# Kernel tuning notes

Hardware: AMD Instinct MI355X
Metric: run time of the kernel (lower is better)

## Reference

```python
import jax, jax.numpy as jnp
import numpy as np

N = 8192          # number of nodes
IN_F = 256        # in_features
OUT_F = 128       # out_features
ALPHA = 0.2       # LeakyReLU negative slope


def setup_inputs() -> dict:
    key = jax.random.key(0)
    k1, k2, k3, k4 = jax.random.split(key, 4)
    h = jax.random.normal(k1, (N, IN_F), dtype=jnp.float32)
    adj = jax.random.randint(k2, (N, N), 0, 2, dtype=jnp.int32)  # dense 0/1 adjacency mask
    W = (jax.random.normal(k3, (IN_F, OUT_F), dtype=jnp.float32) * 0.05)   # W.weight^T
    a = (jax.random.normal(k4, (2 * OUT_F,), dtype=jnp.float32) * 0.05)    # a.weight flattened
    return {"h": h, "adj": adj, "W": W, "a": a}


def reference(h, adj, W, a):
    # Wh = self.W(h): [N, OUT_F]
    Wh = h @ W
    # Original builds an [N, N, 2F] concat tensor then projects with 'a'.
    # Equivalent math: e[i, j] = leaky_relu(Wh[i]@a1 + Wh[j]@a2)
    a1, a2 = a[:OUT_F], a[OUT_F:]
    src = Wh @ a1                                     # [N] per-source score
    dst = Wh @ a2                                     # [N] per-target score
    e = jax.nn.leaky_relu(src[:, None] + dst[None, :], negative_slope=ALPHA)  # [N, N]
    # masked softmax over neighbors (dim=1); adj==0 -> -inf
    e = jnp.where(adj == 0, -jnp.inf, e)
    attention = jax.nn.softmax(e, axis=1)             # [N, N]
    # dropout p=0 in eval-mode reference -> identity
    h_prime = attention @ Wh                          # [N, OUT_F]
    return jax.nn.elu(h_prime)                        # concat=True -> ELU
```

## Files before the change

### kernel.cpp

```cpp
#include <hip/hip_runtime.h>
#include <math.h>

#define N 8192
#define IN_F 256
#define OUT_F 128
#define ALPHA 0.2f
#define JS 8
#define NSTEP 32

typedef _Float16 f16;
typedef __attribute__((ext_vector_type(4))) float f32x4;
typedef __attribute__((ext_vector_type(8))) _Float16 f16x8;
typedef __attribute__((ext_vector_type(4))) _Float16 f16x4;

__global__ __launch_bounds__(256) void k_prep(const float* __restrict__ W,
                                              f16* __restrict__ WT) {
    int idx = blockIdx.x * 256 + threadIdx.x;
    int f = idx >> 8;
    int k = idx & 255;
    WT[idx] = (f16)W[k * OUT_F + f];
}

#define HS 280
__global__ __launch_bounds__(256) void k_wh(const float* __restrict__ h,
                                            const f16* __restrict__ WT,
                                            const float* __restrict__ a,
                                            f16* __restrict__ WhT,
                                            float* __restrict__ src,
                                            float* __restrict__ dst) {
    __shared__ __align__(16) f16 hA[32][HS];
    __shared__ __align__(16) f16 outT[128][40];
    __shared__ float sred[4][32], dred[4][32];

    const int t = threadIdx.x;
    const int i0 = blockIdx.x * 32;
    const int wv = t >> 6, l = t & 63, ln = l & 15, lq = l >> 4;

    {
        const float4* hg = (const float4*)(h + (size_t)i0 * IN_F);
#pragma unroll
        for (int it = 0; it < 8; ++it) {
            int idx = t + it * 256;
            int r = idx >> 6;
            int c4 = (idx & 63) * 4;
            float4 v = hg[idx];
            f16x4 p = { (f16)v.x, (f16)v.y, (f16)v.z, (f16)v.w };
            *(f16x4*)&hA[r][c4] = p;
        }
    }
    __syncthreads();

    f32x4 acc00 = {0.f,0.f,0.f,0.f}, acc01 = {0.f,0.f,0.f,0.f};
    f32x4 acc10 = {0.f,0.f,0.f,0.f}, acc11 = {0.f,0.f,0.f,0.f};
    const int f0 = 32 * wv;

#pragma unroll
    for (int ks = 0; ks < 8; ++ks) {
        const int k0 = 32 * ks + 8 * lq;
        f16x8 a0 = *(const f16x8*)&hA[ln][k0];
        f16x8 a1 = *(const f16x8*)&hA[16 + ln][k0];
        f16x8 b0 = *(const f16x8*)(WT + (size_t)(f0 + ln) * IN_F + k0);
        f16x8 b1 = *(const f16x8*)(WT + (size_t)(f0 + 16 + ln) * IN_F + k0);
        acc00 = __builtin_amdgcn_mfma_f32_16x16x32_f16(a0, b0, acc00, 0, 0, 0);
        acc01 = __builtin_amdgcn_mfma_f32_16x16x32_f16(a0, b1, acc01, 0, 0, 0);
        acc10 = __builtin_amdgcn_mfma_f32_16x16x32_f16(a1, b0, acc10, 0, 0, 0);
        acc11 = __builtin_amdgcn_mfma_f32_16x16x32_f16(a1, b1, acc11, 0, 0, 0);
    }

    const float a1c0 = a[f0 + ln],      a2c0 = a[128 + f0 + ln];
    const float a1c1 = a[f0 + 16 + ln], a2c1 = a[128 + f0 + 16 + ln];
    float sp[8], dp[8];
#pragma unroll
    for (int i = 0; i < 8; ++i) { sp[i] = 0.f; dp[i] = 0.f; }

#pragma unroll
    for (int hh = 0; hh < 2; ++hh) {
        f32x4 v0 = hh ? acc10 : acc00;
        f32x4 v1 = hh ? acc11 : acc01;
        f16x4 p0, p1;
#pragma unroll
        for (int rg = 0; rg < 4; ++rg) {
            sp[hh * 4 + rg] += v0[rg] * a1c0 + v1[rg] * a1c1;
            dp[hh * 4 + rg] += v0[rg] * a2c0 + v1[rg] * a2c1;
            p0[rg] = (f16)v0[rg];
            p1[rg] = (f16)v1[rg];
        }
        *(f16x4*)&outT[f0 + ln][16 * hh + 4 * lq] = p0;
        *(f16x4*)&outT[f0 + 16 + ln][16 * hh + 4 * lq] = p1;
    }
#pragma unroll
    for (int i = 0; i < 8; ++i) {
        float s = sp[i], d = dp[i];
        s += __shfl_down(s, 8, 16); d += __shfl_down(d, 8, 16);
        s += __shfl_down(s, 4, 16); d += __shfl_down(d, 4, 16);
        s += __shfl_down(s, 2, 16); d += __shfl_down(d, 2, 16);
        s += __shfl_down(s, 1, 16); d += __shfl_down(d, 1, 16);
        if (ln == 0) {
            int row = 16 * (i >> 2) + 4 * lq + (i & 3);
            sred[wv][row] = s;
            dred[wv][row] = d;
        }
    }
    __syncthreads();
    if (t < 32) {
        src[i0 + t] = sred[0][t] + sred[1][t] + sred[2][t] + sred[3][t];
        dst[i0 + t] = dred[0][t] + dred[1][t] + dred[2][t] + dred[3][t];
    }
    {
        const int col = t & 127, g = t >> 7;
        const int ct = i0 >> 7, jo = i0 & 127;
        f16x8 q0 = *(const f16x8*)&outT[col][16 * g];
        f16x8 q1 = *(const f16x8*)&outT[col][16 * g + 8];
        f16* dstp = WhT + (size_t)ct * (128 * 128) + (size_t)col * 128 + jo + 16 * g;
        *(f16x8*)(dstp) = q0;
        *(f16x8*)(dstp + 8) = q1;
    }
}

__global__ __launch_bounds__(256, 2) void k_attn(const int* __restrict__ adj,
                                                 const f16* __restrict__ WhT,
                                                 const float* __restrict__ src,
                                                 const float* __restrict__ dst,
                                                 float* __restrict__ p_part,
                                                 float* __restrict__ l_part) {
    const int t = threadIdx.x;
    const int wv = t >> 6, l = t & 63, ln = l & 15, lq = l >> 4;
    const int i0 = (blockIdx.x * 4 + wv) * 32;
    const int jq = blockIdx.y;
    const int jbase = jq * (N / JS);

    const float src0 = src[i0 + ln];
    const float src1 = src[i0 + 16 + ln];
    const float c0 = fabsf(src0) + 4.0f;
    const float c1 = fabsf(src1) + 4.0f;
    float lp0 = 0.f, lp1 = 0.f;

    f32x4 acc0[8], acc1[8];
#pragma unroll
    for (int ft = 0; ft < 8; ++ft) {
        acc0[ft] = (f32x4){0.f,0.f,0.f,0.f};
        acc1[ft] = (f32x4){0.f,0.f,0.f,0.f};
    }

    const int* arow0 = adj + (size_t)(i0 + ln) * N + jbase + 8 * lq;
    const int* arow1 = arow0 + (size_t)16 * N;
    const float* drow = dst + jbase + 8 * lq;
    const f16* Bb = WhT + (size_t)(jq * 8) * (128 * 128) + (size_t)ln * 128 + 8 * lq;

    int4 pa0[2][2], pa1[2][2];
    float4 pd[2][2];

    auto issue = [&](int s, int p) {
        const int off = 32 * (s & (NSTEP - 1));
        pa0[p][0] = *(const int4*)(arow0 + off);
        pa0[p][1] = *(const int4*)(arow0 + off + 4);
        pa1[p][0] = *(const int4*)(arow1 + off);
        pa1[p][1] = *(const int4*)(arow1 + off + 4);
        pd[p][0]  = *(const float4*)(drow + off);
        pd[p][1]  = *(const float4*)(drow + off + 4);
    };

    issue(0, 0);
    issue(1, 1);

#pragma unroll 4
    for (int s = 0; s < NSTEP; ++s) {
        const int p = s & 1;
        const int4 a00 = pa0[p][0], a01 = pa0[p][1];
        const int4 a10 = pa1[p][0], a11 = pa1[p][1];
        const float4 d0 = pd[p][0], d1 = pd[p][1];
        issue(s + 2, p);

        const int* av0 = (const int*)&a00;
        const int* av1 = (const int*)&a01;
        const int* bv0 = (const int*)&a10;
        const int* bv1 = (const int*)&a11;
        const float* df0 = (const float*)&d0;
        const float* df1 = (const float*)&d1;

        f16x8 af0, af1;
#pragma unroll
        for (int k = 0; k < 4; ++k) {
            float e0 = src0 + df0[k];
            float w0 = av0[k] ? __expf(fmaxf(e0, ALPHA * e0) - c0) : 0.f;
            lp0 += w0; af0[k] = (f16)w0;
            float e1 = src1 + df0[k];
            float w1 = bv0[k] ? __expf(fmaxf(e1, ALPHA * e1) - c1) : 0.f;
            lp1 += w1; af1[k] = (f16)w1;
        }
#pragma unroll
        for (int k = 0; k < 4; ++k) {
            float e0 = src0 + df1[k];
            float w0 = av1[k] ? __expf(fmaxf(e0, ALPHA * e0) - c0) : 0.f;
            lp0 += w0; af0[4 + k] = (f16)w0;
            float e1 = src1 + df1[k];
            float w1 = bv1[k] ? __expf(fmaxf(e1, ALPHA * e1) - c1) : 0.f;
            lp1 += w1; af1[4 + k] = (f16)w1;
        }

        const f16* bp = Bb + (s >> 2) * (128 * 128) + (s & 3) * 32;
#pragma unroll
        for (int ft = 0; ft < 8; ++ft) {
            f16x8 bf = *(const f16x8*)(bp + ft * (16 * 128));
            acc0[ft] = __builtin_amdgcn_mfma_f32_16x16x32_f16(af0, bf, acc0[ft], 0, 0, 0);
            acc1[ft] = __builtin_amdgcn_mfma_f32_16x16x32_f16(af1, bf, acc1[ft], 0, 0, 0);
        }
    }

    lp0 += __shfl_down(lp0, 32); lp0 += __shfl_down(lp0, 16);
    lp1 += __shfl_down(lp1, 32); lp1 += __shfl_down(lp1, 16);
    if (l < 16) {
        l_part[(size_t)jq * N + i0 + l] = lp0;
        l_part[(size_t)jq * N + i0 + 16 + l] = lp1;
    }

    float* pb = p_part + (size_t)jq * N * OUT_F;
#pragma unroll
    for (int ft = 0; ft < 8; ++ft) {
#pragma unroll
        for (int rg = 0; rg < 4; ++rg) {
            pb[(size_t)(i0 + 4 * lq + rg) * OUT_F + 16 * ft + ln] = acc0[ft][rg];
            pb[(size_t)(i0 + 16 + 4 * lq + rg) * OUT_F + 16 * ft + ln] = acc1[ft][rg];
        }
    }
}

__global__ __launch_bounds__(256) void k_comb(const float* __restrict__ p_part,
                                              const float* __restrict__ l_part,
                                              float* __restrict__ out) {
    const int idx4 = blockIdx.x * 256 + threadIdx.x;
    const int row = idx4 >> 5;
    const float4* pp = (const float4*)p_part;
    float4 p = pp[idx4];
    float lsum = l_part[row];
#pragma unroll
    for (int q = 1; q < JS; ++q) {
        float4 v = pp[(size_t)q * (N * OUT_F / 4) + idx4];
        p.x += v.x; p.y += v.y; p.z += v.z; p.w += v.w;
        lsum += l_part[(size_t)q * N + row];
    }
    float inv = 1.0f / lsum;
    float4 r;
    r.x = p.x * inv; r.x = r.x > 0.f ? r.x : expm1f(r.x);
    r.y = p.y * inv; r.y = r.y > 0.f ? r.y : expm1f(r.y);
    r.z = p.z * inv; r.z = r.z > 0.f ? r.z : expm1f(r.z);
    r.w = p.w * inv; r.w = r.w > 0.f ? r.w : expm1f(r.w);
    ((float4*)out)[idx4] = r;
}

extern "C" void kernel_launch(void* const* d_in, const int* in_sizes, int n_in,
                              void* d_out, int out_size, void* d_ws, size_t ws_size,
                              hipStream_t stream) {
    const float* h   = (const float*)d_in[0];
    const int*   adj = (const int*)d_in[1];
    const float* W   = (const float*)d_in[2];
    const float* a   = (const float*)d_in[3];
    float* out = (float*)d_out;

    char* ws = (char*)d_ws;
    f16*   WT     = (f16*)ws;                       ws += 64 * 1024;
    f16*   WhT    = (f16*)ws;                       ws += 2 * 1024 * 1024;
    float* src    = (float*)ws;                     ws += N * sizeof(float);
    float* dst    = (float*)ws;                     ws += N * sizeof(float);
    float* l_part = (float*)ws;                     ws += (size_t)JS * N * sizeof(float);
    float* p_part = (float*)ws;

    k_prep<<<128, 256, 0, stream>>>(W, WT);
    k_wh<<<N / 32, 256, 0, stream>>>(h, WT, a, WhT, src, dst);
    dim3 agrid(N / 128, JS);
    k_attn<<<agrid, 256, 0, stream>>>(adj, WhT, src, dst, p_part, l_part);
    k_comb<<<N * OUT_F / 4 / 256, 256, 0, stream>>>(p_part, l_part, out);
}
```

Before: 443.4 us.

## Pack adjacency into bitmask in pre-pass and prefetch WhT fragments in attention loop

Adds a pre-pass kernel that compresses the int32 adjacency matrix into a bitmask, so the attention kernel reads 1 bit per edge instead of 4 bytes. The attention loop now loads mask words per 4-step group and double-buffers the WhT B-fragments in registers one step ahead. The full 256 MB adjacency still has to be read once by the pack kernel, which adds a launch and a workspace buffer. It also raises register pressure in the attention kernel.

```diff
diff --git a/kernel.cpp b/kernel.cpp
--- a/kernel.cpp
+++ b/kernel.cpp
@@ -7,6 +7,7 @@
 #define ALPHA 0.2f
 #define JS 8
 #define NSTEP 32
+#define MW (N / 32)
 
 typedef _Float16 f16;
 typedef __attribute__((ext_vector_type(4))) float f32x4;
@@ -19,6 +20,24 @@
     int f = idx >> 8;
     int k = idx & 255;
     WT[idx] = (f16)W[k * OUT_F + f];
+}
+
+__global__ __launch_bounds__(256) void k_pack(const int* __restrict__ adj,
+                                              unsigned* __restrict__ M) {
+    const int t = threadIdx.x;
+    const int l = t & 63;
+    const size_t tot = (size_t)N * N / 4;
+    const size_t stride = (size_t)gridDim.x * 256;
+    size_t idx = (size_t)blockIdx.x * 256 + t;
+    const int4* ap = (const int4*)adj;
+    for (; idx < tot; idx += stride) {
+        int4 v = ap[idx];
+        unsigned m = (v.x ? 1u : 0u) | (v.y ? 2u : 0u) | (v.z ? 4u : 0u) | (v.w ? 8u : 0u);
+        m |= __shfl_down(m, 1) << 4;
+        m |= __shfl_down(m, 2) << 8;
+        m |= __shfl_down(m, 4) << 16;
+        if ((l & 7) == 0) M[idx >> 3] = m;
+    }
 }
 
 #define HS 280
@@ -117,7 +136,7 @@
     }
 }
 
-__global__ __launch_bounds__(256, 2) void k_attn(const int* __restrict__ adj,
+__global__ __launch_bounds__(256, 2) void k_attn(const unsigned* __restrict__ M,
                                                  const f16* __restrict__ WhT,
                                                  const float* __restrict__ src,
                                                  const float* __restrict__ dst,
@@ -142,69 +161,68 @@
         acc1[ft] = (f32x4){0.f,0.f,0.f,0.f};
     }
 
-    const int* arow0 = adj + (size_t)(i0 + ln) * N + jbase + 8 * lq;
-    const int* arow1 = arow0 + (size_t)16 * N;
+    const unsigned* Mr0 = M + (size_t)(i0 + ln) * MW + jq * (NSTEP);
+    const unsigned* Mr1 = Mr0 + (size_t)16 * MW;
     const float* drow = dst + jbase + 8 * lq;
     const f16* Bb = WhT + (size_t)(jq * 8) * (128 * 128) + (size_t)ln * 128 + 8 * lq;
 
-    int4 pa0[2][2], pa1[2][2];
     float4 pd[2][2];
-
-    auto issue = [&](int s, int p) {
+    auto dissue = [&](int s, int p) {
         const int off = 32 * (s & (NSTEP - 1));
-        pa0[p][0] = *(const int4*)(arow0 + off);
-        pa0[p][1] = *(const int4*)(arow0 + off + 4);
-        pa1[p][0] = *(const int4*)(arow1 + off);
-        pa1[p][1] = *(const int4*)(arow1 + off + 4);
-        pd[p][0]  = *(const float4*)(drow + off);
-        pd[p][1]  = *(const float4*)(drow + off + 4);
+        pd[p][0] = *(const float4*)(drow + off);
+        pd[p][1] = *(const float4*)(drow + off + 4);
     };
-
-    issue(0, 0);
-    issue(1, 1);
-
-#pragma unroll 4
-    for (int s = 0; s < NSTEP; ++s) {
-        const int p = s & 1;
-        const int4 a00 = pa0[p][0], a01 = pa0[p][1];
-        const int4 a10 = pa1[p][0], a11 = pa1[p][1];
-        const float4 d0 = pd[p][0], d1 = pd[p][1];
-        issue(s + 2, p);
-
-        const int* av0 = (const int*)&a00;
-        const int* av1 = (const int*)&a01;
-        const int* bv0 = (const int*)&a10;
-        const int* bv1 = (const int*)&a11;
-        const float* df0 = (const float*)&d0;
-        const float* df1 = (const float*)&d1;
-
-        f16x8 af0, af1;
-#pragma unroll
-        for (int k = 0; k < 4; ++k) {
-            float e0 = src0 + df0[k];
-            float w0 = av0[k] ? __expf(fmaxf(e0, ALPHA * e0) - c0) : 0.f;
-            lp0 += w0; af0[k] = (f16)w0;
-            float e1 = src1 + df0[k];
-            float w1 = bv0[k] ? __expf(fmaxf(e1, ALPHA * e1) - c1) : 0.f;
-            lp1 += w1; af1[k] = (f16)w1;
-        }
-#pragma unroll
-        for (int k = 0; k < 4; ++k) {
-            float e0 = src0 + df1[k];
-            float w0 = av1[k] ? __expf(fmaxf(e0, ALPHA * e0) - c0) : 0.f;
-            lp0 += w0; af0[4 + k] = (f16)w0;
-            float e1 = src1 + df1[k];
-            float w1 = bv1[k] ? __expf(fmaxf(e1, ALPHA * e1) - c1) : 0.f;
-            lp1 += w1; af1[4 + k] = (f16)w1;
-        }
-
-        const f16* bp = Bb + (s >> 2) * (128 * 128) + (s & 3) * 32;
-#pragma unroll
-        for (int ft = 0; ft < 8; ++ft) {
-            f16x8 bf = *(const f16x8*)(bp + ft * (16 * 128));
-            acc0[ft] = __builtin_amdgcn_mfma_f32_16x16x32_f16(af0, bf, acc0[ft], 0, 0, 0);
-            acc1[ft] = __builtin_amdgcn_mfma_f32_16x16x32_f16(af1, bf, acc1[ft], 0, 0, 0);
-        }
+    f16x8 bfb[2][8];
+    auto bissue = [&](int s) {
+        const int ss = s & (NSTEP - 1);
+        const f16* bp = Bb + (ss >> 2) * (128 * 128) + (ss & 3) * 32;
+#pragma unroll
+        for (int ft = 0; ft < 8; ++ft)
+            bfb[s & 1][ft] = *(const f16x8*)(bp + ft * (16 * 128));
+    };
+
+    uint4 m0c = *(const uint4*)Mr0;
+    uint4 m1c = *(const uint4*)Mr1;
+    dissue(0, 0);
+    dissue(1, 1);
+    bissue(0);
+
+    for (int g = 0; g < 8; ++g) {
+        uint4 m0n, m1n;
+        if (g < 7) {
+            m0n = *(const uint4*)(Mr0 + 4 * (g + 1));
+            m1n = *(const uint4*)(Mr1 + 4 * (g + 1));
+        }
+#pragma unroll
+        for (int s4 = 0; s4 < 4; ++s4) {
+            const int s = 4 * g + s4;
+            const int p = s & 1;
+            const float4 d0 = pd[p][0], d1 = pd[p][1];
+            dissue(s + 2, p);
+            bissue(s + 1);
+            const unsigned b0 = (((const unsigned*)&m0c)[s4] >> (8 * lq)) & 0xffu;
+            const unsigned b1 = (((const unsigned*)&m1c)[s4] >> (8 * lq)) & 0xffu;
+            const float* df0 = (const float*)&d0;
+            const float* df1 = (const float*)&d1;
+            f16x8 af0, af1;
+#pragma unroll
+            for (int k = 0; k < 8; ++k) {
+                const float dv = (k < 4) ? df0[k] : df1[k - 4];
+                float e0 = src0 + dv;
+                float w0 = (b0 >> k) & 1u ? __expf(fmaxf(e0, ALPHA * e0) - c0) : 0.f;
+                lp0 += w0; af0[k] = (f16)w0;
+                float e1 = src1 + dv;
+                float w1 = (b1 >> k) & 1u ? __expf(fmaxf(e1, ALPHA * e1) - c1) : 0.f;
+                lp1 += w1; af1[k] = (f16)w1;
+            }
+#pragma unroll
+            for (int ft = 0; ft < 8; ++ft) {
+                f16x8 bf = bfb[p][ft];
+                acc0[ft] = __builtin_amdgcn_mfma_f32_16x16x32_f16(af0, bf, acc0[ft], 0, 0, 0);
+                acc1[ft] = __builtin_amdgcn_mfma_f32_16x16x32_f16(af1, bf, acc1[ft], 0, 0, 0);
+            }
+        }
+        if (g < 7) { m0c = m0n; m1c = m1n; }
     }
 
     lp0 += __shfl_down(lp0, 32); lp0 += __shfl_down(lp0, 16);
@@ -258,16 +276,18 @@
     float* out = (float*)d_out;
 
     char* ws = (char*)d_ws;
-    f16*   WT     = (f16*)ws;                       ws += 64 * 1024;
-    f16*   WhT    = (f16*)ws;                       ws += 2 * 1024 * 1024;
-    float* src    = (float*)ws;                     ws += N * sizeof(float);
-    float* dst    = (float*)ws;                     ws += N * sizeof(float);
-    float* l_part = (float*)ws;                     ws += (size_t)JS * N * sizeof(float);
-    float* p_part = (float*)ws;
-
+    f16*      WT     = (f16*)ws;        ws += 64 * 1024;
+    f16*      WhT    = (f16*)ws;        ws += 2 * 1024 * 1024;
+    float*    src    = (float*)ws;      ws += N * sizeof(float);
+    float*    dst    = (float*)ws;      ws += N * sizeof(float);
+    float*    l_part = (float*)ws;      ws += (size_t)JS * N * sizeof(float);
+    unsigned* M      = (unsigned*)ws;   ws += (size_t)N * MW * sizeof(unsigned);
+    float*    p_part = (float*)ws;
+
+    k_pack<<<2048, 256, 0, stream>>>(adj, M);
     k_prep<<<128, 256, 0, stream>>>(W, WT);
     k_wh<<<N / 32, 256, 0, stream>>>(h, WT, a, WhT, src, dst);
     dim3 agrid(N / 128, JS);
-    k_attn<<<agrid, 256, 0, stream>>>(adj, WhT, src, dst, p_part, l_part);
+    k_attn<<<agrid, 256, 0, stream>>>(M, WhT, src, dst, p_part, l_part);
     k_comb<<<N * OUT_F / 4 / 256, 256, 0, stream>>>(p_part, l_part, out);
 }
```

Result: slower. 488.3 us (+10.1%).
